# Performance work log

Measured on AMD Instinct MI355X. Metric: run time of the kernel, lower is better.

## Reference

```python
import jax, jax.numpy as jnp
import numpy as np
from functools import partial

N_NODES = 50000
N_EDGES = 800000
N_ENT = 100000
N_REL = 500
N_POS = 7            # sub_graph_hop_num + 2
DIM = 128            # node_emb_dim == rel_emb_dim == hidden_dim
HEADS = 8
HEAD_DIM = DIM // HEADS
HOPS = 3             # gnn_hop_num
ALPHA = 0.15
FFN_DIM = 4 * DIM
BATCH = 512
SLOPE = 0.2          # leaky relu negative slope


def _ln(x, g, b):
    mu = jnp.mean(x, axis=-1, keepdims=True)
    var = jnp.var(x, axis=-1, keepdims=True)
    return (x - mu) * jax.lax.rsqrt(var + 1e-5) * g + b


def _gdt_layer(h, src, dst, Wh, ah, at, g1, b1, w1, c1, w2, c2, g2, b2,
               rel_score=None):
    """Graph diffusion-transformer layer: edge-softmax attention + PPR hops."""
    N = h.shape[0]
    f = (h @ Wh).reshape(N, HEADS, HEAD_DIM)          # [N,H,Dh]
    s_src = jnp.sum(f * ah, axis=-1)                  # [N,H]
    s_dst = jnp.sum(f * at, axis=-1)                  # [N,H]
    e = s_src[src] + s_dst[dst]                       # [E,H]
    if rel_score is not None:
        e = e + rel_score
    e = jnp.where(e >= 0, e, SLOPE * e)               # leaky relu
    m = jax.ops.segment_max(e, dst, num_segments=N)   # [N,H]
    m = jnp.where(jnp.isfinite(m), m, 0.0)
    ex = jnp.exp(e - m[dst])
    den = jax.ops.segment_sum(ex, dst, num_segments=N)
    att = ex / (den[dst] + 1e-16)                     # [E,H] edge softmax

    feat0 = f
    def hop(feat, _):
        msg = feat[src] * att[:, :, None]             # [E,H,Dh]
        agg = jax.ops.segment_sum(msg, dst, num_segments=N)
        return ALPHA * feat0 + (1.0 - ALPHA) * agg, None
    feat, _ = jax.lax.scan(hop, feat0, None, length=HOPS)

    o = feat.reshape(N, DIM)
    o = _ln(o + h, g1, b1)                            # residual + LN
    ff = jax.nn.relu(o @ w1 + c1) @ w2 + c2           # FFN
    return _ln(o + ff, g2, b2)


def setup_inputs() -> dict:
    key = jax.random.key(0)
    ks = jax.random.split(key, 32)
    s = 0.05
    inp = {
        'ent_ids': jax.random.randint(ks[0], (N_NODES,), 0, N_ENT),
        'rel_ids': jax.random.randint(ks[1], (N_EDGES,), 0, N_REL),
        'arw_pos': jax.random.randint(ks[2], (N_NODES,), 0, N_POS),
        'src': jax.random.randint(ks[3], (N_EDGES,), 0, N_NODES),
        'dst': jax.random.randint(ks[4], (N_EDGES,), 0, N_NODES),
        'batch_node_ids': jax.random.randint(ks[5], (BATCH,), 0, N_NODES),
        'ent_tab': jax.random.normal(ks[6], (N_ENT, DIM)) * s,
        'rel_tab': jax.random.normal(ks[7], (N_REL, DIM)) * s,
        'pos_tab': jax.random.normal(ks[8], (N_POS, DIM)) * s,
        # layer 0 (RGDT: uses relation features)
        'l0_Wh': jax.random.normal(ks[9], (DIM, DIM)) * s,
        'l0_Wr': jax.random.normal(ks[10], (DIM, DIM)) * s,
        'l0_ah': jax.random.normal(ks[11], (HEADS, HEAD_DIM)) * s,
        'l0_at': jax.random.normal(ks[12], (HEADS, HEAD_DIM)) * s,
        'l0_ar': jax.random.normal(ks[13], (HEADS, HEAD_DIM)) * s,
        'l0_g1': jnp.ones((DIM,)), 'l0_b1': jnp.zeros((DIM,)),
        'l0_w1': jax.random.normal(ks[14], (DIM, FFN_DIM)) * s,
        'l0_c1': jnp.zeros((FFN_DIM,)),
        'l0_w2': jax.random.normal(ks[15], (FFN_DIM, DIM)) * s,
        'l0_c2': jnp.zeros((DIM,)),
        'l0_g2': jnp.ones((DIM,)), 'l0_b2': jnp.zeros((DIM,)),
        # layer 1 (GDT: no relation features)
        'l1_Wh': jax.random.normal(ks[16], (DIM, DIM)) * s,
        'l1_ah': jax.random.normal(ks[17], (HEADS, HEAD_DIM)) * s,
        'l1_at': jax.random.normal(ks[18], (HEADS, HEAD_DIM)) * s,
        'l1_g1': jnp.ones((DIM,)), 'l1_b1': jnp.zeros((DIM,)),
        'l1_w1': jax.random.normal(ks[19], (DIM, FFN_DIM)) * s,
        'l1_c1': jnp.zeros((FFN_DIM,)),
        'l1_w2': jax.random.normal(ks[20], (FFN_DIM, DIM)) * s,
        'l1_c2': jnp.zeros((DIM,)),
        'l1_g2': jnp.ones((DIM,)), 'l1_b2': jnp.zeros((DIM,)),
    }
    return inp


def reference(ent_ids, rel_ids, arw_pos, src, dst, batch_node_ids,
              ent_tab, rel_tab, pos_tab,
              l0_Wh, l0_Wr, l0_ah, l0_at, l0_ar, l0_g1, l0_b1,
              l0_w1, l0_c1, l0_w2, l0_c2, l0_g2, l0_b2,
              l1_Wh, l1_ah, l1_at, l1_g1, l1_b1,
              l1_w1, l1_c1, l1_w2, l1_c2, l1_g2, l1_b2):
    # embedding gathers + positional add
    h = ent_tab[ent_ids] + pos_tab[arw_pos]           # [N,D]
    rel = rel_tab[rel_ids]                            # [E,D]
    # relation contribution to layer-0 attention scores
    fr = (rel @ l0_Wr).reshape(-1, HEADS, HEAD_DIM)
    rel_score = jnp.sum(fr * l0_ar, axis=-1)          # [E,H]
    h = _gdt_layer(h, src, dst, l0_Wh, l0_ah, l0_at, l0_g1, l0_b1,
                   l0_w1, l0_c1, l0_w2, l0_c2, l0_g2, l0_b2,
                   rel_score=rel_score)
    h = _gdt_layer(h, src, dst, l1_Wh, l1_ah, l1_at, l1_g1, l1_b1,
                   l1_w1, l1_c1, l1_w2, l1_c2, l1_g2, l1_b2)
    return h[batch_node_ids]                          # [B,D] cls gather
```

## Files before the change

### kernel.cpp

```cpp
#include <hip/hip_runtime.h>
#include <hip/hip_bf16.h>

#define NNODES 50000
#define NEDGES 800000
#define NP 50048
#define DIM 128
#define HEADS 8
#define FFNDIM 512

typedef __bf16 bf16x8 __attribute__((ext_vector_type(8)));
typedef float f32x4 __attribute__((ext_vector_type(4)));
typedef unsigned int uint32;
typedef unsigned short ushort16;

__device__ __forceinline__ float b2f(uint32 u) {
  union { uint32 i; float f; } x; x.i = u << 16; return x.f;
}
__device__ __forceinline__ ushort16 f2b(float f) {
  __bf16 h = (__bf16)f; return __builtin_bit_cast(ushort16, h);
}
__device__ __forceinline__ float h2f(unsigned short u) {
  return (float)__builtin_bit_cast(_Float16, u);
}
__device__ __forceinline__ unsigned short f2h(float f) {
  return __builtin_bit_cast(unsigned short, (_Float16)f);
}

__global__ void k_embed_hist(const int* __restrict__ ent_ids, const int* __restrict__ arw_pos,
                             const float* __restrict__ ent_tab, const float* __restrict__ pos_tab,
                             __bf16* __restrict__ hb, const int* __restrict__ dst,
                             int* __restrict__ deg) {
  int bid = blockIdx.x, tid = threadIdx.x;
  if (bid < 6250) {
    int t = bid * 256 + tid;
    int n = t >> 5, c = t & 31;
    float4 a = ((const float4*)ent_tab)[ent_ids[n] * 32 + c];
    float4 b = ((const float4*)pos_tab)[arw_pos[n] * 32 + c];
    ushort4 o;
    o.x = f2b(a.x + b.x); o.y = f2b(a.y + b.y);
    o.z = f2b(a.z + b.z); o.w = f2b(a.w + b.w);
    ((ushort4*)hb)[t] = o;
  } else {
    int hbid = bid - 6250;
    int part = hbid & 7;
    int lo = part * 6250, hi2 = lo + 6250;
    for (int e = (hbid >> 3) * 256 + tid; e < NEDGES; e += 256 * 256) {
      int d = dst[e];
      if (d >= lo && d < hi2) atomicAdd(&deg[d], 1);
    }
  }
}

__global__ void k_prep(const int* __restrict__ deg, int* __restrict__ rowptr,
                       int* __restrict__ cursor,
                       const float* __restrict__ Wr, const float* __restrict__ ar,
                       const float* __restrict__ rel_tab, float* __restrict__ relsc,
                       const float* __restrict__ Wh0, const float* __restrict__ Wh1,
                       const float* __restrict__ w10, const float* __restrict__ w11,
                       const float* __restrict__ w20, const float* __restrict__ w21,
                       __bf16* __restrict__ T0, __bf16* __restrict__ T1,
                       __bf16* __restrict__ T2, __bf16* __restrict__ T3,
                       __bf16* __restrict__ T4, __bf16* __restrict__ T5) {
  int bid = blockIdx.x, tid = threadIdx.x;
  if (bid == 0) {
    __shared__ int wsum[16];
    __shared__ int s_run;
    int lane = tid & 63, w = tid >> 6;
    if (tid == 0) s_run = 0;
    __syncthreads();
    for (int base = 0; base < NNODES; base += 1024) {
      int i = base + tid;
      int v = (i < NNODES) ? deg[i] : 0;
      int x = v;
      #pragma unroll
      for (int o = 1; o < 64; o <<= 1) {
        int t = __shfl_up(x, o);
        if (lane >= o) x += t;
      }
      if (lane == 63) wsum[w] = x;
      __syncthreads();
      if (w == 0 && lane < 16) {
        int t = wsum[lane];
        #pragma unroll
        for (int o = 1; o < 16; o <<= 1) {
          int u = __shfl_up(t, o);
          if (lane >= o) t += u;
        }
        wsum[lane] = t;
      }
      __syncthreads();
      int run = s_run;
      int add = run + (w > 0 ? wsum[w - 1] : 0);
      if (i < NNODES) { rowptr[i] = add + x - v; cursor[i] = add + x - v; }
      __syncthreads();
      if (tid == 0) s_run = run + wsum[15];
      __syncthreads();
    }
    if (tid == 0) rowptr[NNODES] = s_run;
  } else if (bid <= 4) {
    __shared__ float vr[1024];
    int d = tid >> 3, hh = tid & 7;
    float s = 0.f;
    #pragma unroll
    for (int k = 0; k < 16; ++k) s += Wr[d * 128 + hh * 16 + k] * ar[hh * 16 + k];
    vr[tid] = s;
    __syncthreads();
    int t = (bid - 1) * 1024 + tid;
    if (t < 500 * 8) {
      int r = t >> 3, h2 = t & 7;
      float acc = 0.f;
      for (int dd = 0; dd < 128; ++dd) acc += rel_tab[r * 128 + dd] * vr[dd * 8 + h2];
      relsc[t] = acc;
    }
  } else {
    int wb = bid - 5;
    const float* W; __bf16* T; int lr2, lc2;
    int sub;
    if (wb < 16)        { W = Wh0; T = T0; lr2 = 7; lc2 = 7; sub = wb; }
    else if (wb < 32)   { W = Wh1; T = T1; lr2 = 7; lc2 = 7; sub = wb - 16; }
    else if (wb < 96)   { W = w10; T = T2; lr2 = 7; lc2 = 9; sub = wb - 32; }
    else if (wb < 160)  { W = w11; T = T3; lr2 = 7; lc2 = 9; sub = wb - 96; }
    else if (wb < 224)  { W = w20; T = T4; lr2 = 9; lc2 = 7; sub = wb - 160; }
    else                { W = w21; T = T5; lr2 = 9; lc2 = 7; sub = wb - 224; }
    int idx = sub * 1024 + tid;
    int r = idx & ((1 << lr2) - 1);
    int c = idx >> lr2;
    T[((long)c << lr2) + r] = (__bf16)W[((long)r << lc2) + c];
  }
}

__global__ __launch_bounds__(256) void k_scatter(
    const int* __restrict__ dst, const int* __restrict__ src,
    const int* __restrict__ rel_ids, int* __restrict__ cursor,
    uint32* __restrict__ packed) {
  int part = blockIdx.x & 7;
  int lo = part * 6250, hi2 = lo + 6250;
  int tid = threadIdx.x;
  for (int e = (int)(blockIdx.x >> 3) * 256 + tid; e < NEDGES; e += 256 * 256) {
    int d = dst[e];
    if (d >= lo && d < hi2) {
      int p = atomicAdd(&cursor[d], 1);
      packed[p] = (uint32)src[e] | ((uint32)rel_ids[e] << 16);
    }
  }
}

__global__ __launch_bounds__(256) void k_gemm0s(
    const __bf16* __restrict__ A, const __bf16* __restrict__ Bt,
    __bf16* __restrict__ fout, const float* __restrict__ ah, const float* __restrict__ at,
    float* __restrict__ ssrc, float* __restrict__ sdst) {
  __shared__ char sA[16384];
  __shared__ char sB[16384];
  const int tid = threadIdx.x;
  const int lane = tid & 63, wid = tid >> 6;
  const int wr = wid >> 1, wc = wid & 1;
  const int lr = lane & 15, hi = lane >> 4;
  const long row0 = (long)blockIdx.x * 128;
  f32x4 acc[4][4] = {};

  for (int kc = 0; kc < 2; ++kc) {
    __syncthreads();
    #pragma unroll
    for (int i = 0; i < 4; ++i) {
      int q = i * 256 + tid;
      int r = q >> 3, slot = q & 7;
      int sw = ((slot ^ (r & 7)) << 4);
      int4 av = *(const int4*)(A + (row0 + r) * 128 + kc * 64 + slot * 8);
      *(int4*)(sA + r * 128 + sw) = av;
      int4 bv = *(const int4*)(Bt + (long)r * 128 + kc * 64 + slot * 8);
      *(int4*)(sB + r * 128 + sw) = bv;
    }
    __syncthreads();
    #pragma unroll
    for (int ks = 0; ks < 2; ++ks) {
      bf16x8 af[4], bfr[4];
      #pragma unroll
      for (int m = 0; m < 4; ++m) {
        int r = wr * 64 + m * 16 + lr;
        int cb = ((ks * 4 + hi) ^ (r & 7)) << 4;
        af[m] = *(const bf16x8*)(sA + r * 128 + cb);
      }
      #pragma unroll
      for (int n = 0; n < 4; ++n) {
        int r = wc * 64 + n * 16 + lr;
        int cb = ((ks * 4 + hi) ^ (r & 7)) << 4;
        bfr[n] = *(const bf16x8*)(sB + r * 128 + cb);
      }
      #pragma unroll
      for (int m = 0; m < 4; ++m)
        #pragma unroll
        for (int n = 0; n < 4; ++n)
          acc[m][n] = __builtin_amdgcn_mfma_f32_16x16x32_bf16(af[m], bfr[n], acc[m][n], 0, 0, 0);
    }
  }

  float ahr[4], atr[4];
  #pragma unroll
  for (int n = 0; n < 4; ++n) {
    ahr[n] = ah[(wc * 4 + n) * 16 + lr];
    atr[n] = at[(wc * 4 + n) * 16 + lr];
  }
  #pragma unroll
  for (int m = 0; m < 4; ++m) {
    #pragma unroll
    for (int j = 0; j < 4; ++j) {
      long r = row0 + wr * 64 + m * 16 + hi * 4 + j;
      #pragma unroll
      for (int n = 0; n < 4; ++n) {
        long c = wc * 64 + n * 16 + lr;
        float v = acc[m][n][j];
        fout[r * 128 + c] = (__bf16)v;
        float ps = v * ahr[n], pt = v * atr[n];
        #pragma unroll
        for (int o = 1; o < 16; o <<= 1) { ps += __shfl_xor(ps, o); pt += __shfl_xor(pt, o); }
        if (lr == 0) {
          ssrc[r * 8 + wc * 4 + n] = ps;
          sdst[r * 8 + wc * 4 + n] = pt;
        }
      }
    }
  }
}

template<int KDIM, int NB>
__global__ __launch_bounds__(256) void k_gemm(
    const __bf16* __restrict__ A, const __bf16* __restrict__ Bt,
    const float* __restrict__ bias, __bf16* __restrict__ outb) {
  __shared__ char sA[16384];
  __shared__ char sB[16384];
  const int tid = threadIdx.x;
  const int lane = tid & 63, wid = tid >> 6;
  const int wr = wid >> 1, wc = wid & 1;
  const int lr = lane & 15, hi = lane >> 4;
  const long row0 = (long)blockIdx.x * 128;
  const long col0 = (long)blockIdx.y * 128;
  f32x4 acc[4][4] = {};

  for (int kc = 0; kc < KDIM / 64; ++kc) {
    __syncthreads();
    #pragma unroll
    for (int i = 0; i < 4; ++i) {
      int q = i * 256 + tid;
      int r = q >> 3, slot = q & 7;
      int sw = ((slot ^ (r & 7)) << 4);
      int4 av = *(const int4*)(A + (row0 + r) * KDIM + kc * 64 + slot * 8);
      *(int4*)(sA + r * 128 + sw) = av;
      int4 bv = *(const int4*)(Bt + (col0 + r) * KDIM + kc * 64 + slot * 8);
      *(int4*)(sB + r * 128 + sw) = bv;
    }
    __syncthreads();
    #pragma unroll
    for (int ks = 0; ks < 2; ++ks) {
      bf16x8 af[4], bfr[4];
      #pragma unroll
      for (int m = 0; m < 4; ++m) {
        int r = wr * 64 + m * 16 + lr;
        int cb = ((ks * 4 + hi) ^ (r & 7)) << 4;
        af[m] = *(const bf16x8*)(sA + r * 128 + cb);
      }
      #pragma unroll
      for (int n = 0; n < 4; ++n) {
        int r = wc * 64 + n * 16 + lr;
        int cb = ((ks * 4 + hi) ^ (r & 7)) << 4;
        bfr[n] = *(const bf16x8*)(sB + r * 128 + cb);
      }
      #pragma unroll
      for (int m = 0; m < 4; ++m)
        #pragma unroll
        for (int n = 0; n < 4; ++n)
          acc[m][n] = __builtin_amdgcn_mfma_f32_16x16x32_bf16(af[m], bfr[n], acc[m][n], 0, 0, 0);
    }
  }

  #pragma unroll
  for (int m = 0; m < 4; ++m) {
    #pragma unroll
    for (int j = 0; j < 4; ++j) {
      long r = row0 + wr * 64 + m * 16 + hi * 4 + j;
      #pragma unroll
      for (int n = 0; n < 4; ++n) {
        long c = col0 + wc * 64 + n * 16 + lr;
        outb[r * NB + c] = (__bf16)fmaxf(acc[m][n][j] + bias[c], 0.f);
      }
    }
  }
}

__global__ __launch_bounds__(256) void k_gemm2ln(
    const __bf16* __restrict__ A, const __bf16* __restrict__ Bt,
    const float* __restrict__ bias, const __bf16* __restrict__ resid,
    const float* __restrict__ g, const float* __restrict__ b,
    __bf16* __restrict__ outb, float* __restrict__ outf) {
  __shared__ char smem[65536];
  char* sA = smem;
  char* sB = smem + 16384;
  float* sV = (float*)smem;
  const int tid = threadIdx.x;
  const int lane = tid & 63, wid = tid >> 6;
  const int wr = wid >> 1, wc = wid & 1;
  const int lr = lane & 15, hi = lane >> 4;
  const long row0 = (long)blockIdx.x * 128;
  f32x4 acc[4][4] = {};

  for (int kc = 0; kc < 8; ++kc) {
    __syncthreads();
    #pragma unroll
    for (int i = 0; i < 4; ++i) {
      int q = i * 256 + tid;
      int r = q >> 3, slot = q & 7;
      int sw = ((slot ^ (r & 7)) << 4);
      int4 av = *(const int4*)(A + (row0 + r) * 512 + kc * 64 + slot * 8);
      *(int4*)(sA + r * 128 + sw) = av;
      int4 bv = *(const int4*)(Bt + (long)r * 512 + kc * 64 + slot * 8);
      *(int4*)(sB + r * 128 + sw) = bv;
    }
    __syncthreads();
    #pragma unroll
    for (int ks = 0; ks < 2; ++ks) {
      bf16x8 af[4], bfr[4];
      #pragma unroll
      for (int m = 0; m < 4; ++m) {
        int r = wr * 64 + m * 16 + lr;
        int cb = ((ks * 4 + hi) ^ (r & 7)) << 4;
        af[m] = *(const bf16x8*)(sA + r * 128 + cb);
      }
      #pragma unroll
      for (int n = 0; n < 4; ++n) {
        int r = wc * 64 + n * 16 + lr;
        int cb = ((ks * 4 + hi) ^ (r & 7)) << 4;
        bfr[n] = *(const bf16x8*)(sB + r * 128 + cb);
      }
      #pragma unroll
      for (int m = 0; m < 4; ++m)
        #pragma unroll
        for (int n = 0; n < 4; ++n)
          acc[m][n] = __builtin_amdgcn_mfma_f32_16x16x32_bf16(af[m], bfr[n], acc[m][n], 0, 0, 0);
    }
  }
  __syncthreads();

  float biasr[4];
  #pragma unroll
  for (int n = 0; n < 4; ++n) biasr[n] = bias[wc * 64 + n * 16 + lr];
  #pragma unroll
  for (int m = 0; m < 4; ++m) {
    #pragma unroll
    for (int j = 0; j < 4; ++j) {
      int rloc = wr * 64 + m * 16 + hi * 4 + j;
      long r = row0 + rloc;
      #pragma unroll
      for (int n = 0; n < 4; ++n) {
        int c = wc * 64 + n * 16 + lr;
        sV[rloc * 128 + c] = acc[m][n][j] + biasr[n] + (float)resid[r * 128 + c];
      }
    }
  }
  __syncthreads();

  float2 gg = ((const float2*)g)[lane];
  float2 bb = ((const float2*)b)[lane];
  for (int rr = 0; rr < 32; ++rr) {
    int rloc = wid * 32 + rr;
    long r = row0 + rloc;
    float2 v = ((float2*)sV)[rloc * 64 + lane];
    float x = v.x, y = v.y;
    float s = x + y;
    #pragma unroll
    for (int o = 1; o < 64; o <<= 1) s += __shfl_xor(s, o);
    float mean = s * (1.f / 128.f);
    float dx = x - mean, dy = y - mean;
    float q = dx * dx + dy * dy;
    #pragma unroll
    for (int o = 1; o < 64; o <<= 1) q += __shfl_xor(q, o);
    float rs = rsqrtf(q * (1.f / 128.f) + 1e-5f);
    float ox = dx * rs * gg.x + bb.x;
    float oy = dy * rs * gg.y + bb.y;
    if (outf) ((float2*)outf)[r * 64 + lane] = make_float2(ox, oy);
    ((uint32*)outb)[r * 64 + lane] = ((uint32)f2b(oy) << 16) | (uint32)f2b(ox);
  }
}

__global__ void k_softmax(const int* __restrict__ rowptr, const uint32* __restrict__ packed,
                          const float* __restrict__ ssrc, const float* __restrict__ sdst,
                          const float* __restrict__ relsc, unsigned short* __restrict__ att16) {
  int lane = threadIdx.x & 63, wid = threadIdx.x >> 6;
  int n = blockIdx.x * 4 + wid;
  if (n >= NNODES) return;
  int start = rowptr[n], end = rowptr[n + 1];
  if (start == end) return;
  int hh = lane & 7, jj = lane >> 3;
  float sd = sdst[n * 8 + hh];
  float m = -1e30f, den = 0.f;
  int deg = end - start;

  if (deg <= 64) {
    uint32 pk[8];
    float ev[8];
    int end1 = end - 1;
    #pragma unroll
    for (int t = 0; t < 8; ++t)
      pk[t] = packed[min(start + t * 8 + jj, end1)];
    #pragma unroll
    for (int t = 0; t < 8; ++t)
      ev[t] = ssrc[(pk[t] & 0xffffu) * 8 + hh];
    #pragma unroll
    for (int t = 0; t < 8; ++t) {
      int j = start + t * 8 + jj;
      float e = ev[t] + sd;
      if (relsc) e += relsc[(pk[t] >> 16) * 8 + hh];
      e = (e >= 0.f) ? e : 0.2f * e;
      ev[t] = e;
      if (j < end) {
        float M = fmaxf(m, e);
        den = den * __expf(m - M) + __expf(e - M);
        m = M;
      }
    }
    #pragma unroll
    for (int o = 8; o < 64; o <<= 1) {
      float m2 = __shfl_xor(m, o), d2 = __shfl_xor(den, o);
      float M = fmaxf(m, m2);
      den = den * __expf(m - M) + d2 * __expf(m2 - M);
      m = M;
    }
    float inv = 1.f / (den + 1e-16f);
    #pragma unroll
    for (int t = 0; t < 8; ++t) {
      int j = start + t * 8 + jj;
      if (j < end) att16[j * 8 + hh] = f2h(__expf(ev[t] - m) * inv);
    }
  } else {
    for (int j0 = start; j0 < end; j0 += 8) {
      int j = j0 + jj;
      if (j < end) {
        uint32 p2 = packed[j];
        float e = ssrc[(p2 & 0xffffu) * 8 + hh] + sd;
        if (relsc) e += relsc[(p2 >> 16) * 8 + hh];
        e = (e >= 0.f) ? e : 0.2f * e;
        att16[j * 8 + hh] = f2h(e);
        float M = fmaxf(m, e);
        den = den * __expf(m - M) + __expf(e - M);
        m = M;
      }
    }
    #pragma unroll
    for (int o = 8; o < 64; o <<= 1) {
      float m2 = __shfl_xor(m, o), d2 = __shfl_xor(den, o);
      float M = fmaxf(m, m2);
      den = den * __expf(m - M) + d2 * __expf(m2 - M);
      m = M;
    }
    float inv = 1.f / (den + 1e-16f);
    for (int j0 = start; j0 < end; j0 += 8) {
      int j = j0 + jj;
      if (j < end) att16[j * 8 + hh] = f2h(__expf(h2f(att16[j * 8 + hh]) - m) * inv);
    }
  }
}

template<int FINAL>
__global__ __launch_bounds__(256) void k_hop(
    const int* __restrict__ rowptr, const uint32* __restrict__ packed,
    const unsigned short* __restrict__ att16, const __bf16* __restrict__ fin,
    const __bf16* __restrict__ f0, __bf16* __restrict__ fout,
    const __bf16* __restrict__ resid, const float* __restrict__ g,
    const float* __restrict__ b) {
  int lane = threadIdx.x & 63, wid = threadIdx.x >> 6;
  int n = blockIdx.x * 4 + wid;
  if (n >= NNODES) return;
  int start = rowptr[n], end = rowptr[n + 1];
  int hsel = lane >> 3, hsel2 = lane >> 4, hlo = hsel & 1;
  float ax = 0.f, ay = 0.f;
  const uint32* fin2 = (const uint32*)fin;
  const uint32* au = (const uint32*)att16;
  if (start < end) {
    int end1 = end - 1, limit4 = end * 4 - 1;
    uint32 sv = packed[min(start + (lane & 31), end1)];
    uint32 a0 = au[min(start * 4 + lane, limit4)];
    uint32 a1 = au[min(start * 4 + 64 + lane, limit4)];
    for (int j0 = start; j0 < end; j0 += 32) {
      uint32 svc = sv, b0 = a0, b1 = a1;
      int jn = j0 + 32;
      if (jn < end) {
        sv = packed[min(jn + (lane & 31), end1)];
        a0 = au[min(jn * 4 + lane, limit4)];
        a1 = au[min(jn * 4 + 64 + lane, limit4)];
      }
      #pragma unroll
      for (int k = 0; k < 32; ++k) {
        uint32 araw = __shfl((k < 16) ? b0 : b1, ((k & 15) << 2) + hsel2);
        unsigned short hu = hlo ? (unsigned short)(araw >> 16)
                                : (unsigned short)(araw & 0xffffu);
        float a = h2f(hu);
        a = (j0 + k < end) ? a : 0.f;
        int s = (int)(__shfl(svc, k) & 0xffffu);
        uint32 v = fin2[(long)s * 64 + lane];
        ax += a * b2f(v & 0xffffu);
        ay += a * b2f(v >> 16);
      }
    }
  }
  uint32 z = ((const uint32*)f0)[n * 64 + lane];
  float ox = 0.15f * b2f(z & 0xffffu) + 0.85f * ax;
  float oy = 0.15f * b2f(z >> 16) + 0.85f * ay;
  if (!FINAL) {
    ((uint32*)fout)[n * 64 + lane] = ((uint32)f2b(oy) << 16) | (uint32)f2b(ox);
  } else {
    uint32 rz = ((const uint32*)resid)[n * 64 + lane];
    float x = ox + b2f(rz & 0xffffu);
    float y = oy + b2f(rz >> 16);
    float s = x + y;
    #pragma unroll
    for (int o = 1; o < 64; o <<= 1) s += __shfl_xor(s, o);
    float mean = s * (1.f / 128.f);
    float dx = x - mean, dy = y - mean;
    float q = dx * dx + dy * dy;
    #pragma unroll
    for (int o = 1; o < 64; o <<= 1) q += __shfl_xor(q, o);
    float rs2 = rsqrtf(q * (1.f / 128.f) + 1e-5f);
    float2 gg = ((const float2*)g)[lane];
    float2 bb = ((const float2*)b)[lane];
    float o1 = dx * rs2 * gg.x + bb.x;
    float o2 = dy * rs2 * gg.y + bb.y;
    ((uint32*)fout)[n * 64 + lane] = ((uint32)f2b(o2) << 16) | (uint32)f2b(o1);
  }
}

__global__ void k_gather(const int* __restrict__ ids, const float* __restrict__ h,
                         float* __restrict__ out) {
  int t = blockIdx.x * 256 + threadIdx.x;
  if (t >= 512 * 32) return;
  int b = t >> 5, c = t & 31;
  ((float4*)out)[t] = ((const float4*)h)[(long)ids[b] * 32 + c];
}

struct LayerW {
  const float *Wh, *ah, *at, *g1, *b1, *w1, *c1, *w2, *c2, *g2, *b2;
};

extern "C" void kernel_launch(void* const* d_in, const int* in_sizes, int n_in,
                              void* d_out, int out_size, void* d_ws, size_t ws_size,
                              hipStream_t stream) {
  const int* ent_ids   = (const int*)d_in[0];
  const int* rel_ids   = (const int*)d_in[1];
  const int* arw_pos   = (const int*)d_in[2];
  const int* src       = (const int*)d_in[3];
  const int* dst       = (const int*)d_in[4];
  const int* batch_ids = (const int*)d_in[5];
  const float* ent_tab = (const float*)d_in[6];
  const float* rel_tab = (const float*)d_in[7];
  const float* pos_tab = (const float*)d_in[8];

  LayerW L0 = {(const float*)d_in[9],  (const float*)d_in[11], (const float*)d_in[12],
               (const float*)d_in[14], (const float*)d_in[15], (const float*)d_in[16],
               (const float*)d_in[17], (const float*)d_in[18], (const float*)d_in[19],
               (const float*)d_in[20], (const float*)d_in[21]};
  const float* l0_Wr = (const float*)d_in[10];
  const float* l0_ar = (const float*)d_in[13];
  LayerW L1 = {(const float*)d_in[22], (const float*)d_in[23], (const float*)d_in[24],
               (const float*)d_in[25], (const float*)d_in[26], (const float*)d_in[27],
               (const float*)d_in[28], (const float*)d_in[29], (const float*)d_in[30],
               (const float*)d_in[31], (const float*)d_in[32]};

  char* p = (char*)d_ws;
  auto alloc = [&](size_t bytes) { char* q = p; p += (bytes + 255) & ~(size_t)255; return q; };
  __bf16* hb = (__bf16*)alloc((size_t)NP * 128 * 2);
  __bf16* f  = (__bf16*)alloc((size_t)NP * 128 * 2);
  __bf16* fb = (__bf16*)alloc((size_t)NP * 128 * 2);
  __bf16* fa = (__bf16*)alloc((size_t)NP * 128 * 2);
  __bf16* ob = (__bf16*)alloc((size_t)NP * 128 * 2);
  char*   U  = alloc((size_t)NP * 512 * 2);
  unsigned short* att16 = (unsigned short*)U;
  __bf16* T   = (__bf16*)U;
  float*  y   = (float*)f;
  float* ssrc  = (float*)alloc((size_t)NP * 8 * 4);
  float* sdst  = (float*)alloc((size_t)NP * 8 * 4);
  float* relsc = (float*)alloc(500 * 8 * 4);
  __bf16* Wht0 = (__bf16*)alloc(128 * 128 * 2);
  __bf16* Wht1 = (__bf16*)alloc(128 * 128 * 2);
  __bf16* w1t0 = (__bf16*)alloc(512 * 128 * 2);
  __bf16* w1t1 = (__bf16*)alloc(512 * 128 * 2);
  __bf16* w2t0 = (__bf16*)alloc(128 * 512 * 2);
  __bf16* w2t1 = (__bf16*)alloc(128 * 512 * 2);
  int* deg    = (int*)alloc(NNODES * 4);
  int* rowptr = (int*)alloc((NNODES + 1) * 4);
  int* cursor = (int*)alloc(NNODES * 4);
  uint32* packed = (uint32*)alloc((size_t)NEDGES * 4);

  hipMemsetAsync(hb + (size_t)NNODES * 128, 0, (size_t)(NP - NNODES) * 128 * 2, stream);
  hipMemsetAsync(ob + (size_t)NNODES * 128, 0, (size_t)(NP - NNODES) * 128 * 2, stream);
  hipMemsetAsync(deg, 0, NNODES * sizeof(int), stream);

  k_embed_hist<<<6250 + 2048, 256, 0, stream>>>(ent_ids, arw_pos, ent_tab, pos_tab, hb, dst, deg);
  k_prep<<<293, 1024, 0, stream>>>(deg, rowptr, cursor, l0_Wr, l0_ar, rel_tab, relsc,
                                   L0.Wh, L1.Wh, L0.w1, L1.w1, L0.w2, L1.w2,
                                   Wht0, Wht1, w1t0, w1t1, w2t0, w2t1);
  k_scatter<<<2048, 256, 0, stream>>>(dst, src, rel_ids, cursor, packed);

  const int NB4 = (NNODES + 3) / 4;
  for (int L = 0; L < 2; ++L) {
    const LayerW& W = L ? L1 : L0;
    const __bf16* Wht = L ? Wht1 : Wht0;
    const __bf16* w1t = L ? w1t1 : w1t0;
    const __bf16* w2t = L ? w2t1 : w2t0;
    const float* rsc  = L ? nullptr : relsc;

    k_gemm0s<<<391, 256, 0, stream>>>(hb, Wht, f, W.ah, W.at, ssrc, sdst);
    k_softmax<<<NB4, 256, 0, stream>>>(rowptr, packed, ssrc, sdst, rsc, att16);
    k_hop<0><<<NB4, 256, 0, stream>>>(rowptr, packed, att16, f, f, fa, nullptr, nullptr, nullptr);
    k_hop<0><<<NB4, 256, 0, stream>>>(rowptr, packed, att16, fa, f, fb, nullptr, nullptr, nullptr);
    k_hop<1><<<NB4, 256, 0, stream>>>(rowptr, packed, att16, fb, f, ob, hb, W.g1, W.b1);
    k_gemm<128, 512><<<dim3(391, 4), 256, 0, stream>>>(ob, w1t, W.c1, T);
    k_gemm2ln<<<391, 256, 0, stream>>>(T, w2t, W.c2, ob, W.g2, W.b2, hb,
                                       (L == 1) ? y : nullptr);
  }

  k_gather<<<64, 256, 0, stream>>>(batch_ids, y, (float*)d_out);
}
```

Baseline: 596.0 us.

## Pre-shift packed source indices, store fp32 attention, restructure hop loop

Packs source node ids pre-multiplied by the row stride (src<<6) and relation ids at bit 22, so gather addresses need only an OR with the lane. Attention weights are stored as fp32 instead of fp16, removing half-precision conversions and shuffle unpacking in the hop kernel. The hop loop now processes full 16-edge chunks with prefetch plus a scalar tail loop, replacing masked 32-edge chunks. This doubles attention-buffer traffic, and the serial tail may add latency for the many low-degree nodes.

```diff
diff --git a/kernel.cpp b/kernel.cpp
--- a/kernel.cpp
+++ b/kernel.cpp
@@ -16,14 +16,11 @@
 __device__ __forceinline__ float b2f(uint32 u) {
   union { uint32 i; float f; } x; x.i = u << 16; return x.f;
 }
+__device__ __forceinline__ float b2fh(uint32 u) {
+  union { uint32 i; float f; } x; x.i = u & 0xffff0000u; return x.f;
+}
 __device__ __forceinline__ ushort16 f2b(float f) {
   __bf16 h = (__bf16)f; return __builtin_bit_cast(ushort16, h);
-}
-__device__ __forceinline__ float h2f(unsigned short u) {
-  return (float)__builtin_bit_cast(_Float16, u);
-}
-__device__ __forceinline__ unsigned short f2h(float f) {
-  return __builtin_bit_cast(unsigned short, (_Float16)f);
 }
 
 __global__ void k_embed_hist(const int* __restrict__ ent_ids, const int* __restrict__ arw_pos,
@@ -140,7 +137,7 @@
     int d = dst[e];
     if (d >= lo && d < hi2) {
       int p = atomicAdd(&cursor[d], 1);
-      packed[p] = (uint32)src[e] | ((uint32)rel_ids[e] << 16);
+      packed[p] = ((uint32)src[e] << 6) | ((uint32)rel_ids[e] << 22);
     }
   }
 }
@@ -382,7 +379,7 @@
 
 __global__ void k_softmax(const int* __restrict__ rowptr, const uint32* __restrict__ packed,
                           const float* __restrict__ ssrc, const float* __restrict__ sdst,
-                          const float* __restrict__ relsc, unsigned short* __restrict__ att16) {
+                          const float* __restrict__ relsc, float* __restrict__ att) {
   int lane = threadIdx.x & 63, wid = threadIdx.x >> 6;
   int n = blockIdx.x * 4 + wid;
   if (n >= NNODES) return;
@@ -402,12 +399,12 @@
       pk[t] = packed[min(start + t * 8 + jj, end1)];
     #pragma unroll
     for (int t = 0; t < 8; ++t)
-      ev[t] = ssrc[(pk[t] & 0xffffu) * 8 + hh];
+      ev[t] = ssrc[((pk[t] & 0x3fffffu) >> 3) | (uint32)hh];
     #pragma unroll
     for (int t = 0; t < 8; ++t) {
       int j = start + t * 8 + jj;
       float e = ev[t] + sd;
-      if (relsc) e += relsc[(pk[t] >> 16) * 8 + hh];
+      if (relsc) e += relsc[((pk[t] >> 22) << 3) | (uint32)hh];
       e = (e >= 0.f) ? e : 0.2f * e;
       ev[t] = e;
       if (j < end) {
@@ -427,17 +424,17 @@
     #pragma unroll
     for (int t = 0; t < 8; ++t) {
       int j = start + t * 8 + jj;
-      if (j < end) att16[j * 8 + hh] = f2h(__expf(ev[t] - m) * inv);
+      if (j < end) att[j * 8 + hh] = __expf(ev[t] - m) * inv;
     }
   } else {
     for (int j0 = start; j0 < end; j0 += 8) {
       int j = j0 + jj;
       if (j < end) {
         uint32 p2 = packed[j];
-        float e = ssrc[(p2 & 0xffffu) * 8 + hh] + sd;
-        if (relsc) e += relsc[(p2 >> 16) * 8 + hh];
+        float e = ssrc[((p2 & 0x3fffffu) >> 3) | (uint32)hh] + sd;
+        if (relsc) e += relsc[((p2 >> 22) << 3) | (uint32)hh];
         e = (e >= 0.f) ? e : 0.2f * e;
-        att16[j * 8 + hh] = f2h(e);
+        att[j * 8 + hh] = e;
         float M = fmaxf(m, e);
         den = den * __expf(m - M) + __expf(e - M);
         m = M;
@@ -453,7 +450,7 @@
     float inv = 1.f / (den + 1e-16f);
     for (int j0 = start; j0 < end; j0 += 8) {
       int j = j0 + jj;
-      if (j < end) att16[j * 8 + hh] = f2h(__expf(h2f(att16[j * 8 + hh]) - m) * inv);
+      if (j < end) att[j * 8 + hh] = __expf(att[j * 8 + hh] - m) * inv;
     }
   }
 }
@@ -461,7 +458,7 @@
 template<int FINAL>
 __global__ __launch_bounds__(256) void k_hop(
     const int* __restrict__ rowptr, const uint32* __restrict__ packed,
-    const unsigned short* __restrict__ att16, const __bf16* __restrict__ fin,
+    const float* __restrict__ att, const __bf16* __restrict__ fin,
     const __bf16* __restrict__ f0, __bf16* __restrict__ fout,
     const __bf16* __restrict__ resid, const float* __restrict__ g,
     const float* __restrict__ b) {
@@ -469,46 +466,49 @@
   int n = blockIdx.x * 4 + wid;
   if (n >= NNODES) return;
   int start = rowptr[n], end = rowptr[n + 1];
-  int hsel = lane >> 3, hsel2 = lane >> 4, hlo = hsel & 1;
+  int hsel = lane >> 3;
   float ax = 0.f, ay = 0.f;
   const uint32* fin2 = (const uint32*)fin;
-  const uint32* au = (const uint32*)att16;
-  if (start < end) {
-    int end1 = end - 1, limit4 = end * 4 - 1;
-    uint32 sv = packed[min(start + (lane & 31), end1)];
-    uint32 a0 = au[min(start * 4 + lane, limit4)];
-    uint32 a1 = au[min(start * 4 + 64 + lane, limit4)];
-    for (int j0 = start; j0 < end; j0 += 32) {
-      uint32 svc = sv, b0 = a0, b1 = a1;
-      int jn = j0 + 32;
-      if (jn < end) {
-        sv = packed[min(jn + (lane & 31), end1)];
-        a0 = au[min(jn * 4 + lane, limit4)];
-        a1 = au[min(jn * 4 + 64 + lane, limit4)];
-      }
-      #pragma unroll
-      for (int k = 0; k < 32; ++k) {
-        uint32 araw = __shfl((k < 16) ? b0 : b1, ((k & 15) << 2) + hsel2);
-        unsigned short hu = hlo ? (unsigned short)(araw >> 16)
-                                : (unsigned short)(araw & 0xffffu);
-        float a = h2f(hu);
-        a = (j0 + k < end) ? a : 0.f;
-        int s = (int)(__shfl(svc, k) & 0xffffu);
-        uint32 v = fin2[(long)s * 64 + lane];
+  int jend = start + ((end - start) & ~15);
+  if (start < jend) {
+    uint32 sv = packed[start + (lane & 15)];
+    float av0 = att[start * 8 + lane];
+    float av1 = att[start * 8 + 64 + lane];
+    for (int j0 = start; j0 < jend; j0 += 16) {
+      uint32 svc = sv; float a0 = av0, a1 = av1;
+      int jn = j0 + 16;
+      if (jn < jend) {
+        sv = packed[jn + (lane & 15)];
+        av0 = att[jn * 8 + lane];
+        av1 = att[jn * 8 + 64 + lane];
+      }
+      #pragma unroll
+      for (int k = 0; k < 16; ++k) {
+        float a = (k < 8) ? __shfl(a0, k * 8 + hsel) : __shfl(a1, (k - 8) * 8 + hsel);
+        uint32 idx = (__shfl(svc, k) & 0x3fffffu) | (uint32)lane;
+        uint32 v = fin2[idx];
         ax += a * b2f(v & 0xffffu);
-        ay += a * b2f(v >> 16);
-      }
-    }
+        ay += a * b2fh(v);
+      }
+    }
+  }
+  for (int j = jend; j < end; ++j) {
+    uint32 pk = packed[j];
+    float a = att[j * 8 + hsel];
+    uint32 idx = (pk & 0x3fffffu) | (uint32)lane;
+    uint32 v = fin2[idx];
+    ax += a * b2f(v & 0xffffu);
+    ay += a * b2fh(v);
   }
   uint32 z = ((const uint32*)f0)[n * 64 + lane];
   float ox = 0.15f * b2f(z & 0xffffu) + 0.85f * ax;
-  float oy = 0.15f * b2f(z >> 16) + 0.85f * ay;
+  float oy = 0.15f * b2fh(z) + 0.85f * ay;
   if (!FINAL) {
     ((uint32*)fout)[n * 64 + lane] = ((uint32)f2b(oy) << 16) | (uint32)f2b(ox);
   } else {
     uint32 rz = ((const uint32*)resid)[n * 64 + lane];
     float x = ox + b2f(rz & 0xffffu);
-    float y = oy + b2f(rz >> 16);
+    float y = oy + b2fh(rz);
     float s = x + y;
     #pragma unroll
     for (int o = 1; o < 64; o <<= 1) s += __shfl_xor(s, o);
@@ -570,7 +570,7 @@
   __bf16* fa = (__bf16*)alloc((size_t)NP * 128 * 2);
   __bf16* ob = (__bf16*)alloc((size_t)NP * 128 * 2);
   char*   U  = alloc((size_t)NP * 512 * 2);
-  unsigned short* att16 = (unsigned short*)U;
+  float*  att = (float*)U;
   __bf16* T   = (__bf16*)U;
   float*  y   = (float*)f;
   float* ssrc  = (float*)alloc((size_t)NP * 8 * 4);
@@ -606,10 +606,10 @@
     const float* rsc  = L ? nullptr : relsc;
 
     k_gemm0s<<<391, 256, 0, stream>>>(hb, Wht, f, W.ah, W.at, ssrc, sdst);
-    k_softmax<<<NB4, 256, 0, stream>>>(rowptr, packed, ssrc, sdst, rsc, att16);
-    k_hop<0><<<NB4, 256, 0, stream>>>(rowptr, packed, att16, f, f, fa, nullptr, nullptr, nullptr);
-    k_hop<0><<<NB4, 256, 0, stream>>>(rowptr, packed, att16, fa, f, fb, nullptr, nullptr, nullptr);
-    k_hop<1><<<NB4, 256, 0, stream>>>(rowptr, packed, att16, fb, f, ob, hb, W.g1, W.b1);
+    k_softmax<<<NB4, 256, 0, stream>>>(rowptr, packed, ssrc, sdst, rsc, att);
+    k_hop<0><<<NB4, 256, 0, stream>>>(rowptr, packed, att, f, f, fa, nullptr, nullptr, nullptr);
+    k_hop<0><<<NB4, 256, 0, stream>>>(rowptr, packed, att, fa, f, fb, nullptr, nullptr, nullptr);
+    k_hop<1><<<NB4, 256, 0, stream>>>(rowptr, packed, att, fb, f, ob, hb, W.g1, W.b1);
     k_gemm<128, 512><<<dim3(391, 4), 256, 0, stream>>>(ob, w1t, W.c1, T);
     k_gemm2ln<<<391, 256, 0, stream>>>(T, w2t, W.c2, ob, W.g2, W.b2, hb,
                                        (L == 1) ? y : nullptr);
```

Measured after the change: 698.9 us. 1.17x slower.
